# Kernel tuning notes

Measured on AMD Instinct MI355X. Metric: run time of the kernel, lower is better.

## Reference

```python
import jax, jax.numpy as jnp
import numpy as np

B, D, T, H = 1024, 128, 256, 64  # batch, input_dim, seq_len, hidden_dim


def _lstm_layer(x_proj, w_hh):
    """x_proj: [B, T, 4H] precomputed input projection (incl. both biases).
    Returns (all hidden states [B, T, H], final hidden [B, H])."""
    b = x_proj.shape[0]
    h0 = jnp.zeros((b, H), x_proj.dtype)
    c0 = jnp.zeros((b, H), x_proj.dtype)

    def step(carry, xt):
        h, c = carry
        gates = xt + h @ w_hh.T  # [B, 4H]; PyTorch gate order i, f, g, o
        i, f, g, o = jnp.split(gates, 4, axis=-1)
        i = jax.nn.sigmoid(i)
        f = jax.nn.sigmoid(f)
        g = jnp.tanh(g)
        o = jax.nn.sigmoid(o)
        c = f * c + i * g
        h = o * jnp.tanh(c)
        return (h, c), h

    (hT, _), ys = jax.lax.scan(step, (h0, c0), x_proj.transpose(1, 0, 2))
    return ys.transpose(1, 0, 2), hT


def setup_inputs() -> dict:
    key = jax.random.key(0)
    ks = jax.random.split(key, 11)
    s = 1.0 / np.sqrt(H)  # PyTorch LSTM init scale
    return {
        "x": jax.random.normal(ks[0], (B, D, T), jnp.float32),
        "w_ih0": jax.random.normal(ks[1], (4 * H, D), jnp.float32) * s,
        "w_hh0": jax.random.normal(ks[2], (4 * H, H), jnp.float32) * s,
        "b_ih0": jax.random.normal(ks[3], (4 * H,), jnp.float32) * s,
        "b_hh0": jax.random.normal(ks[4], (4 * H,), jnp.float32) * s,
        "w_ih1": jax.random.normal(ks[5], (4 * H, H), jnp.float32) * s,
        "w_hh1": jax.random.normal(ks[6], (4 * H, H), jnp.float32) * s,
        "b_ih1": jax.random.normal(ks[7], (4 * H,), jnp.float32) * s,
        "b_hh1": jax.random.normal(ks[8], (4 * H,), jnp.float32) * s,
        "w_fc": jax.random.normal(ks[9], (D, H), jnp.float32) * s,
        "b_fc": jax.random.normal(ks[10], (D,), jnp.float32) * s,
    }


def reference(x, w_ih0, w_hh0, b_ih0, b_hh0, w_ih1, w_hh1, b_ih1, b_hh1, w_fc, b_fc):
    # x: [B, input_dim, T] -> permute(0, 2, 1) -> [B, T, input_dim]
    xt = x.transpose(0, 2, 1)
    # Layer 0: precompute input projection for all timesteps (one big GEMM)
    xp0 = xt @ w_ih0.T + (b_ih0 + b_hh0)  # [B, T, 4H]
    ys0, _ = _lstm_layer(xp0, w_hh0)
    # Inter-layer dropout(p=0.3) is identity in eval/inference mode.
    xp1 = ys0 @ w_ih1.T + (b_ih1 + b_hh1)  # [B, T, 4H]
    _, hT = _lstm_layer(xp1, w_hh1)
    # Final-timestep linear head: lstm_out[:, -1, :] == final hidden state hT
    scores = hT @ w_fc.T + b_fc  # [B, input_dim]
    return scores
```

## Files before the change

### kernel.cpp

```cpp
#include <hip/hip_runtime.h>

#define T_SEQ 256
#define PH  72
#define HSZ 1152
#define XRW 144
#define XSL 584

typedef float f32x4 __attribute__((ext_vector_type(4)));
typedef _Float16 f16x8 __attribute__((ext_vector_type(8)));

__device__ __forceinline__ float sigmoid_f(float x) {
    float e = __builtin_amdgcn_exp2f(-1.4426950408889634f * x);
    return __builtin_amdgcn_rcpf(1.0f + e);
}
__device__ __forceinline__ float tanh_f(float x) {
    float e = __builtin_amdgcn_exp2f(-2.8853900817779268f * x);
    return 2.0f * __builtin_amdgcn_rcpf(1.0f + e) - 1.0f;
}
__device__ __forceinline__ f16x8 load_frag16h(const float* wp, int n, int K, int k0) {
    const float* wf = wp + (size_t)n * K + k0;
    f16x8 h;
    #pragma unroll
    for (int j = 0; j < 8; ++j) h[j] = (_Float16)wf[j];
    return h;
}
__device__ __forceinline__ void load_frag16(const float* wp, int n, int K, int k0,
                                            f16x8& hi, f16x8& lo) {
    const float* wf = wp + (size_t)n * K + k0;
    #pragma unroll
    for (int j = 0; j < 8; ++j) {
        const float v = wf[j];
        const _Float16 h = (_Float16)v;
        hi[j] = h;
        lo[j] = (_Float16)(v - (float)h);
    }
}
__device__ __forceinline__ void gload16(const void* g, void* l) {
    __builtin_amdgcn_global_load_lds(
        (const __attribute__((address_space(1))) unsigned int*)g,
        (__attribute__((address_space(3))) unsigned int*)l, 16, 0, 0);
}

#define MFMA16(a, b, c) __builtin_amdgcn_mfma_f32_16x16x32_f16(a, b, c, 0, 0, 0)

__global__ __launch_bounds__(512, 2) void rec_fused(
    const float* __restrict__ x,
    const float* __restrict__ wih0, const float* __restrict__ whh0,
    const float* __restrict__ bih0, const float* __restrict__ bhh0,
    const float* __restrict__ wih1, const float* __restrict__ whh1,
    const float* __restrict__ bih1, const float* __restrict__ bhh1,
    const float* __restrict__ wfc,  const float* __restrict__ bfc,
    float* __restrict__ out)
{
    __shared__ float    xs32[4 * 2048];
    __shared__ _Float16 xh[32 * XSL];
    __shared__ _Float16 h0[2 * HSZ], h1[2 * HSZ];
    const int tid = threadIdx.x, lane = tid & 63, w = tid >> 6;
    const int l16 = lane & 15, quad = lane >> 4, k0 = quad * 8;
    const int wl = w & 3;
    const bool is1 = (w < 4);
    const int bb  = blockIdx.x & 63;
    const int sub = blockIdx.x >> 6;

    const float* xrow = x + (size_t)(bb * 16 + wl * 4 + sub) * 128 * 256;

    f16x8 fA[4][2], fAl[4][2], fB[4][4];
    float gb[4];
    #pragma unroll
    for (int g = 0; g < 4; ++g) {
        const int n = g * 64 + wl * 16 + l16;
        if (is1) {
            #pragma unroll
            for (int ks = 0; ks < 2; ++ks) {
                fA[g][ks] = load_frag16h(wih1, n, 64, ks * 32 + k0);
                load_frag16(whh1, n, 64, ks * 32 + k0, fB[g][ks], fB[g][2 + ks]);
            }
            gb[g] = bih1[n] + bhh1[n];
        } else {
            #pragma unroll
            for (int ks = 0; ks < 4; ++ks)
                fB[g][ks] = load_frag16h(wih0, n, 128, ks * 32 + k0);
            #pragma unroll
            for (int ks = 0; ks < 2; ++ks)
                load_frag16(whh0, n, 64, ks * 32 + k0, fA[g][ks], fAl[g][ks]);
            gb[g] = bih0[n] + bhh0[n];
        }
    }
    for (int i = tid; i < 2 * HSZ; i += 512) { h0[i] = (_Float16)0.f; h1[i] = (_Float16)0.f; }
    float c = 0.f;

    auto convert_chunk = [&](int cc) {
        const int sb = (cc & 1) * 16;
        const int tq = lane & 3;
        #pragma unroll
        for (int ib = 0; ib < 8; ++ib) {
            const float4 v = *(const float4*)&xs32[wl * 2048 + ib * 256 + lane * 4];
            const int d = ib * 16 + (lane >> 2);
            const float vv[4] = {v.x, v.y, v.z, v.w};
            #pragma unroll
            for (int j = 0; j < 4; ++j)
                xh[(sb + tq * 4 + j) * XSL + wl * XRW + d] = (_Float16)vv[j];
        }
    };
    auto issue_chunk = [&](int cc) {
        #pragma unroll
        for (int ib = 0; ib < 8; ++ib)
            gload16(xrow + (size_t)(ib * 16 + (lane >> 2)) * 256 + cc * 16 + (lane & 3) * 4,
                    (char*)xs32 + wl * 8192 + ib * 1024);
    };

    if (!is1) issue_chunk(0);
    __syncthreads();
    if (!is1) { convert_chunk(0); issue_chunk(1); }
    __syncthreads();

    if (!is1) {
        f16x8 ax[4];
        #pragma unroll
        for (int ks = 0; ks < 4; ++ks)
            ax[ks] = *(const f16x8*)&xh[(l16 >> 2) * XRW + ks * 32 + k0];
        f32x4 acc[4];
        #pragma unroll
        for (int g = 0; g < 4; ++g) acc[g] = (f32x4){gb[g], 0.f, 0.f, 0.f};
        #pragma unroll
        for (int g = 0; g < 4; ++g)
            #pragma unroll
            for (int ks = 0; ks < 4; ++ks)
                acc[g] = MFMA16(ax[ks], fB[g][ks], acc[g]);
        const float gi = sigmoid_f(acc[0][0]);
        const float gg = tanh_f(acc[2][0]);
        const float go = sigmoid_f(acc[3][0]);
        c = gi * gg;
        h0[(quad * 4) * PH + wl * 16 + l16] = (_Float16)(go * tanh_f(c));
    }
    __syncthreads();

    for (int t = 0; t < 255; ++t) {
        const int s0 = t & 1, s1 = s0 ^ 1;
        const int tn = t + 1;
        if (is1) {
            f16x8 ah[2], bh[2];
            #pragma unroll
            for (int ks = 0; ks < 2; ++ks) {
                ah[ks] = *(const f16x8*)&h0[s0 * HSZ + l16 * PH + ks * 32 + k0];
                bh[ks] = *(const f16x8*)&h1[s1 * HSZ + l16 * PH + ks * 32 + k0];
            }
            f32x4 acc[4];
            #pragma unroll
            for (int g = 0; g < 4; ++g)
                acc[g] = (f32x4){gb[g], 0.f, 0.f, 0.f};
            #pragma unroll
            for (int g = 0; g < 4; ++g)
                #pragma unroll
                for (int ks = 0; ks < 2; ++ks) {
                    acc[g] = MFMA16(ah[ks], fA[g][ks], acc[g]);
                    acc[g] = MFMA16(bh[ks], fB[g][ks], acc[g]);
                    acc[g] = MFMA16(bh[ks], fB[g][2 + ks], acc[g]);
                }
            const float gi = sigmoid_f(acc[0][0]);
            const float gf = sigmoid_f(acc[1][0]);
            const float gg = tanh_f(acc[2][0]);
            const float go = sigmoid_f(acc[3][0]);
            c = gf * c + gi * gg;
            h1[s0 * HSZ + (quad * 4) * PH + wl * 16 + l16] =
                (_Float16)(go * tanh_f(c));
        } else {
            if ((tn & 15) == 0 && tn < 240)
                issue_chunk((tn >> 4) + 1);
            const int slot = ((tn >> 4) & 1) * 16 + (tn & 15);
            f16x8 ax[4], ah[2];
            #pragma unroll
            for (int ks = 0; ks < 4; ++ks)
                ax[ks] = *(const f16x8*)&xh[slot * XSL + (l16 >> 2) * XRW + ks * 32 + k0];
            #pragma unroll
            for (int ks = 0; ks < 2; ++ks)
                ah[ks] = *(const f16x8*)&h0[s0 * HSZ + l16 * PH + ks * 32 + k0];
            f32x4 acc[4];
            #pragma unroll
            for (int g = 0; g < 4; ++g) acc[g] = (f32x4){gb[g], 0.f, 0.f, 0.f};
            #pragma unroll
            for (int g = 0; g < 4; ++g) {
                #pragma unroll
                for (int ks = 0; ks < 4; ++ks)
                    acc[g] = MFMA16(ax[ks], fB[g][ks], acc[g]);
                #pragma unroll
                for (int ks = 0; ks < 2; ++ks) {
                    acc[g] = MFMA16(ah[ks], fA[g][ks], acc[g]);
                    acc[g] = MFMA16(ah[ks], fAl[g][ks], acc[g]);
                }
            }
            const float gi = sigmoid_f(acc[0][0]);
            const float gf = sigmoid_f(acc[1][0]);
            const float gg = tanh_f(acc[2][0]);
            const float go = sigmoid_f(acc[3][0]);
            c = gf * c + gi * gg;
            h0[s1 * HSZ + (quad * 4) * PH + wl * 16 + l16] =
                (_Float16)(go * tanh_f(c));
            if ((tn & 15) == 8 && tn < 248)
                convert_chunk((tn >> 4) + 1);
        }
        __syncthreads();
    }

    if (is1) {
        f16x8 ah[2], bh[2];
        #pragma unroll
        for (int ks = 0; ks < 2; ++ks) {
            ah[ks] = *(const f16x8*)&h0[HSZ + l16 * PH + ks * 32 + k0];
            bh[ks] = *(const f16x8*)&h1[l16 * PH + ks * 32 + k0];
        }
        f32x4 acc[4];
        #pragma unroll
        for (int g = 0; g < 4; ++g)
            acc[g] = (f32x4){gb[g], 0.f, 0.f, 0.f};
        #pragma unroll
        for (int g = 0; g < 4; ++g)
            #pragma unroll
            for (int ks = 0; ks < 2; ++ks) {
                acc[g] = MFMA16(ah[ks], fA[g][ks], acc[g]);
                acc[g] = MFMA16(bh[ks], fB[g][ks], acc[g]);
                acc[g] = MFMA16(bh[ks], fB[g][2 + ks], acc[g]);
            }
        const float gi = sigmoid_f(acc[0][0]);
        const float gf = sigmoid_f(acc[1][0]);
        const float gg = tanh_f(acc[2][0]);
        const float go = sigmoid_f(acc[3][0]);
        c = gf * c + gi * gg;
        h1[HSZ + (quad * 4) * PH + wl * 16 + l16] = (_Float16)(go * tanh_f(c));
    }
    __syncthreads();

    const int n   = tid & 127;
    const int sel = tid >> 7;
    float s = 0.f;
    for (int k = 0; k < 64; ++k)
        s += (float)h1[HSZ + (sel * 4) * PH + k] * wfc[n * 64 + k];
    out[(size_t)(bb * 16 + sel * 4 + sub) * 128 + n] = s + bfc[n];
}

extern "C" void kernel_launch(void* const* d_in, const int* in_sizes, int n_in,
                              void* d_out, int out_size, void* d_ws, size_t ws_size,
                              hipStream_t stream) {
    const float* x     = (const float*)d_in[0];
    const float* wih0  = (const float*)d_in[1];
    const float* whh0  = (const float*)d_in[2];
    const float* bih0  = (const float*)d_in[3];
    const float* bhh0  = (const float*)d_in[4];
    const float* wih1  = (const float*)d_in[5];
    const float* whh1  = (const float*)d_in[6];
    const float* bih1  = (const float*)d_in[7];
    const float* bhh1  = (const float*)d_in[8];
    const float* wfc   = (const float*)d_in[9];
    const float* bfc   = (const float*)d_in[10];
    float* out = (float*)d_out;

    rec_fused<<<256, 512, 0, stream>>>(x, wih0, whh0, bih0, bhh0,
                                       wih1, whh1, bih1, bhh1, wfc, bfc, out);
}
```

Before: 370.0 us.

## Precompute next-step input projection off the recurrent critical path, split accumulator chains

Layer-0 waves now compute the x·W_ih MFMA contribution for the next timestep after writing h, so each step only runs the recurrent h·W_hh MFMAs before the gate nonlinearities. The fp32-to-fp16 chunk conversion is spread over four steps instead of one, to even out per-step work. Layer-1 waves split their MFMA dependency chain into two independent accumulators that are summed at the end, shortening the serial MFMA latency. The cost is extra live registers for xacc and the split accumulators, which may reduce occupancy or cause spills.

```diff
diff --git a/kernel.cpp b/kernel.cpp
--- a/kernel.cpp
+++ b/kernel.cpp
@@ -88,12 +88,12 @@
     }
     for (int i = tid; i < 2 * HSZ; i += 512) { h0[i] = (_Float16)0.f; h1[i] = (_Float16)0.f; }
     float c = 0.f;
-
-    auto convert_chunk = [&](int cc) {
+    f32x4 xacc[4];
+
+    auto convert_rows = [&](int cc, int ib0, int nib) {
         const int sb = (cc & 1) * 16;
         const int tq = lane & 3;
-        #pragma unroll
-        for (int ib = 0; ib < 8; ++ib) {
+        for (int ib = ib0; ib < ib0 + nib; ++ib) {
             const float4 v = *(const float4*)&xs32[wl * 2048 + ib * 256 + lane * 4];
             const int d = ib * 16 + (lane >> 2);
             const float vv[4] = {v.x, v.y, v.z, v.w};
@@ -108,30 +108,33 @@
             gload16(xrow + (size_t)(ib * 16 + (lane >> 2)) * 256 + cc * 16 + (lane & 3) * 4,
                     (char*)xs32 + wl * 8192 + ib * 1024);
     };
+    auto precompute_x = [&](int slot) {
+        f16x8 ax[4];
+        #pragma unroll
+        for (int ks = 0; ks < 4; ++ks)
+            ax[ks] = *(const f16x8*)&xh[slot * XSL + (l16 >> 2) * XRW + ks * 32 + k0];
+        #pragma unroll
+        for (int g = 0; g < 4; ++g) xacc[g] = (f32x4){gb[g], 0.f, 0.f, 0.f};
+        #pragma unroll
+        for (int g = 0; g < 4; ++g)
+            #pragma unroll
+            for (int ks = 0; ks < 4; ++ks)
+                xacc[g] = MFMA16(ax[ks], fB[g][ks], xacc[g]);
+    };
 
     if (!is1) issue_chunk(0);
     __syncthreads();
-    if (!is1) { convert_chunk(0); issue_chunk(1); }
+    if (!is1) { convert_rows(0, 0, 8); issue_chunk(1); }
     __syncthreads();
 
     if (!is1) {
-        f16x8 ax[4];
-        #pragma unroll
-        for (int ks = 0; ks < 4; ++ks)
-            ax[ks] = *(const f16x8*)&xh[(l16 >> 2) * XRW + ks * 32 + k0];
-        f32x4 acc[4];
-        #pragma unroll
-        for (int g = 0; g < 4; ++g) acc[g] = (f32x4){gb[g], 0.f, 0.f, 0.f};
-        #pragma unroll
-        for (int g = 0; g < 4; ++g)
-            #pragma unroll
-            for (int ks = 0; ks < 4; ++ks)
-                acc[g] = MFMA16(ax[ks], fB[g][ks], acc[g]);
-        const float gi = sigmoid_f(acc[0][0]);
-        const float gg = tanh_f(acc[2][0]);
-        const float go = sigmoid_f(acc[3][0]);
+        precompute_x(0);
+        const float gi = sigmoid_f(xacc[0][0]);
+        const float gg = tanh_f(xacc[2][0]);
+        const float go = sigmoid_f(xacc[3][0]);
         c = gi * gg;
         h0[(quad * 4) * PH + wl * 16 + l16] = (_Float16)(go * tanh_f(c));
+        precompute_x(1);
     }
     __syncthreads();
 
@@ -145,50 +148,44 @@
                 ah[ks] = *(const f16x8*)&h0[s0 * HSZ + l16 * PH + ks * 32 + k0];
                 bh[ks] = *(const f16x8*)&h1[s1 * HSZ + l16 * PH + ks * 32 + k0];
             }
-            f32x4 acc[4];
-            #pragma unroll
-            for (int g = 0; g < 4; ++g)
-                acc[g] = (f32x4){gb[g], 0.f, 0.f, 0.f};
+            f32x4 accA[4], accB[4];
+            #pragma unroll
+            for (int g = 0; g < 4; ++g) {
+                accA[g] = (f32x4){gb[g], 0.f, 0.f, 0.f};
+                accB[g] = (f32x4){0.f, 0.f, 0.f, 0.f};
+            }
             #pragma unroll
             for (int g = 0; g < 4; ++g)
                 #pragma unroll
                 for (int ks = 0; ks < 2; ++ks) {
-                    acc[g] = MFMA16(ah[ks], fA[g][ks], acc[g]);
-                    acc[g] = MFMA16(bh[ks], fB[g][ks], acc[g]);
-                    acc[g] = MFMA16(bh[ks], fB[g][2 + ks], acc[g]);
+                    accA[g] = MFMA16(ah[ks], fA[g][ks], accA[g]);
+                    accA[g] = MFMA16(bh[ks], fB[g][ks], accA[g]);
+                    accB[g] = MFMA16(bh[ks], fB[g][2 + ks], accB[g]);
                 }
-            const float gi = sigmoid_f(acc[0][0]);
-            const float gf = sigmoid_f(acc[1][0]);
-            const float gg = tanh_f(acc[2][0]);
-            const float go = sigmoid_f(acc[3][0]);
+            const float gi = sigmoid_f(accA[0][0] + accB[0][0]);
+            const float gf = sigmoid_f(accA[1][0] + accB[1][0]);
+            const float gg = tanh_f(accA[2][0] + accB[2][0]);
+            const float go = sigmoid_f(accA[3][0] + accB[3][0]);
             c = gf * c + gi * gg;
             h1[s0 * HSZ + (quad * 4) * PH + wl * 16 + l16] =
                 (_Float16)(go * tanh_f(c));
         } else {
             if ((tn & 15) == 0 && tn < 240)
                 issue_chunk((tn >> 4) + 1);
-            const int slot = ((tn >> 4) & 1) * 16 + (tn & 15);
-            f16x8 ax[4], ah[2];
-            #pragma unroll
-            for (int ks = 0; ks < 4; ++ks)
-                ax[ks] = *(const f16x8*)&xh[slot * XSL + (l16 >> 2) * XRW + ks * 32 + k0];
+            f16x8 ah[2];
             #pragma unroll
             for (int ks = 0; ks < 2; ++ks)
                 ah[ks] = *(const f16x8*)&h0[s0 * HSZ + l16 * PH + ks * 32 + k0];
             f32x4 acc[4];
             #pragma unroll
-            for (int g = 0; g < 4; ++g) acc[g] = (f32x4){gb[g], 0.f, 0.f, 0.f};
-            #pragma unroll
-            for (int g = 0; g < 4; ++g) {
-                #pragma unroll
-                for (int ks = 0; ks < 4; ++ks)
-                    acc[g] = MFMA16(ax[ks], fB[g][ks], acc[g]);
+            for (int g = 0; g < 4; ++g) acc[g] = xacc[g];
+            #pragma unroll
+            for (int g = 0; g < 4; ++g)
                 #pragma unroll
                 for (int ks = 0; ks < 2; ++ks) {
                     acc[g] = MFMA16(ah[ks], fA[g][ks], acc[g]);
                     acc[g] = MFMA16(ah[ks], fAl[g][ks], acc[g]);
                 }
-            }
             const float gi = sigmoid_f(acc[0][0]);
             const float gf = sigmoid_f(acc[1][0]);
             const float gg = tanh_f(acc[2][0]);
@@ -196,8 +193,13 @@
             c = gf * c + gi * gg;
             h0[s1 * HSZ + (quad * 4) * PH + wl * 16 + l16] =
                 (_Float16)(go * tanh_f(c));
-            if ((tn & 15) == 8 && tn < 248)
-                convert_chunk((tn >> 4) + 1);
+            const int m16 = tn & 15;
+            if (m16 >= 8 && m16 < 12 && tn < 248)
+                convert_rows((tn >> 4) + 1, (m16 - 8) * 2, 2);
+            if (tn < 255) {
+                const int tn2 = tn + 1;
+                precompute_x(((tn2 >> 4) & 1) * 16 + (tn2 & 15));
+            }
         }
         __syncthreads();
     }
@@ -209,22 +211,24 @@
             ah[ks] = *(const f16x8*)&h0[HSZ + l16 * PH + ks * 32 + k0];
             bh[ks] = *(const f16x8*)&h1[l16 * PH + ks * 32 + k0];
         }
-        f32x4 acc[4];
+        f32x4 accA[4], accB[4];
+        #pragma unroll
+        for (int g = 0; g < 4; ++g) {
+            accA[g] = (f32x4){gb[g], 0.f, 0.f, 0.f};
+            accB[g] = (f32x4){0.f, 0.f, 0.f, 0.f};
+        }
         #pragma unroll
         for (int g = 0; g < 4; ++g)
-            acc[g] = (f32x4){gb[g], 0.f, 0.f, 0.f};
-        #pragma unroll
-        for (int g = 0; g < 4; ++g)
             #pragma unroll
             for (int ks = 0; ks < 2; ++ks) {
-                acc[g] = MFMA16(ah[ks], fA[g][ks], acc[g]);
-                acc[g] = MFMA16(bh[ks], fB[g][ks], acc[g]);
-                acc[g] = MFMA16(bh[ks], fB[g][2 + ks], acc[g]);
-            }
-        const float gi = sigmoid_f(acc[0][0]);
-        const float gf = sigmoid_f(acc[1][0]);
-        const float gg = tanh_f(acc[2][0]);
-        const float go = sigmoid_f(acc[3][0]);
+                accA[g] = MFMA16(ah[ks], fA[g][ks], accA[g]);
+                accA[g] = MFMA16(bh[ks], fB[g][ks], accA[g]);
+                accB[g] = MFMA16(bh[ks], fB[g][2 + ks], accB[g]);
+            }
+        const float gi = sigmoid_f(accA[0][0] + accB[0][0]);
+        const float gf = sigmoid_f(accA[1][0] + accB[1][0]);
+        const float gg = tanh_f(accA[2][0] + accB[2][0]);
+        const float go = sigmoid_f(accA[3][0] + accB[3][0]);
         c = gf * c + gi * gg;
         h1[HSZ + (quad * 4) * PH + wl * 16 + l16] = (_Float16)(go * tanh_f(c));
     }
```

Measured after the change: 381.4 us. 1.03x slower.
